# Kernel tuning notes

Hardware: AMD Instinct MI355X
Metric: run time of the kernel (lower is better)

The kernel has to match this reference:

```python
import jax, jax.numpy as jnp
import numpy as np

B, S, D = 2, 4096, 2048
HEADS, HEAD_DIM = 16, 128
EPS = 1e-5


def setup_inputs() -> dict:
    key = jax.random.key(0)
    ks = jax.random.split(key, 8)
    hidden_states = jax.random.normal(ks[0], (B, S, D), dtype=jnp.float32)
    # rotary angles, broadcastable to [B, S, heads, head_dim]
    freqs_cis = jax.random.uniform(ks[1], (1, S, 1, HEAD_DIM), dtype=jnp.float32) * 6.283185
    scale = 1.0 / np.sqrt(D)
    # weights stored [in, out] (transpose of torch Linear weight)
    wq = jax.random.normal(ks[2], (D, HEADS * HEAD_DIM), dtype=jnp.float32) * scale
    wk = jax.random.normal(ks[3], (D, HEADS * HEAD_DIM), dtype=jnp.float32) * scale
    wv = jax.random.normal(ks[4], (D, HEADS * HEAD_DIM), dtype=jnp.float32) * scale
    norm_q_w = jnp.ones((HEAD_DIM,), dtype=jnp.float32)
    norm_k_w = jnp.ones((HEAD_DIM,), dtype=jnp.float32)
    w_out = jax.random.normal(ks[5], (HEADS * HEAD_DIM, D), dtype=jnp.float32) * scale
    b_out = jnp.zeros((D,), dtype=jnp.float32)
    return {"hidden_states": hidden_states, "freqs_cis": freqs_cis,
            "wq": wq, "wk": wk, "wv": wv,
            "norm_q_w": norm_q_w, "norm_k_w": norm_k_w,
            "w_out": w_out, "b_out": b_out}


def _rms_norm(x, w):
    var = jnp.mean(jnp.square(x), axis=-1, keepdims=True)
    return x * jax.lax.rsqrt(var + EPS) * w


def _apply_rotary(x, freqs_cis):
    rot_dim = freqs_cis.shape[-1]
    xr, x_pass = x[..., :rot_dim], x[..., rot_dim:]
    cos_ = jnp.cos(freqs_cis).astype(x.dtype)
    sin_ = jnp.sin(freqs_cis).astype(x.dtype)
    x1, x2 = jnp.split(xr, 2, axis=-1)
    x_rot = jnp.concatenate((-x2, x1), axis=-1)
    return jnp.concatenate((xr * cos_ + x_rot * sin_, x_pass), axis=-1)


def reference(hidden_states, freqs_cis, wq, wk, wv, norm_q_w, norm_k_w, w_out, b_out):
    b, s, _ = hidden_states.shape
    # QKV projections -> [B, S, H, Dh]
    q = (hidden_states @ wq).reshape(b, s, HEADS, HEAD_DIM)
    k = (hidden_states @ wk).reshape(b, s, HEADS, HEAD_DIM)
    v = (hidden_states @ wv).reshape(b, s, HEADS, HEAD_DIM)
    q = _rms_norm(q, norm_q_w)
    k = _rms_norm(k, norm_k_w)
    q = _apply_rotary(q, freqs_cis)
    k = _apply_rotary(k, freqs_cis)
    # SDPA with BSND layout, scale = 1/sqrt(head_dim)
    attn = jax.nn.dot_product_attention(q, k, v)  # [B, S, H, Dh]
    out = attn.reshape(b, s, HEADS * HEAD_DIM) @ w_out + b_out
    return out
```

## Files before the change

kernel.cpp:

```cpp
#include <hip/hip_runtime.h>
#include <stdint.h>


#define S_LEN  4096
#define NHEAD  16
#define HDIM   128
#define DMODEL 2048
#define MROWS  8192

typedef unsigned short u16;
typedef unsigned int   u32;
typedef __attribute__((ext_vector_type(4)))  float  f32x4;
typedef __attribute__((ext_vector_type(16))) float  f32x16;
typedef __attribute__((ext_vector_type(4)))  u16    u16x4;
typedef __attribute__((ext_vector_type(8)))  u16    u16x8;
typedef __attribute__((ext_vector_type(4)))  u32    u32x4;
typedef __attribute__((ext_vector_type(8)))  __bf16 bf16x8;

__device__ __forceinline__ u16 f2bf(float x){
  unsigned u = __builtin_bit_cast(unsigned, x);
  u += 0x7FFFu + ((u >> 16) & 1u);
  return (u16)(u >> 16);
}
__device__ __forceinline__ float bf2f(u16 b){
  unsigned u = ((unsigned)b) << 16;
  return __builtin_bit_cast(float, u);
}
__device__ __forceinline__ u32 cvtpk(float lo, float hi_){
  u32 r;
  asm("v_cvt_pk_bf16_f32 %0, %1, %2" : "=v"(r) : "v"(lo), "v"(hi_));
  return r;
}
__device__ __forceinline__ void gload16(const void* g, void* l){
  __builtin_amdgcn_global_load_lds((__attribute__((address_space(1))) void*)g,
                                   (__attribute__((address_space(3))) void*)l,
                                   16, 0, 0);
}
__device__ __forceinline__ int xcd_chunk(int bid, int nwg){
  return (bid & 7) * (nwg >> 3) + (bid >> 3);
}

__global__ void k_cast_hs(const float* __restrict__ in, u16* __restrict__ out){
  size_t i = (size_t)blockIdx.x * 256 + threadIdx.x;
  const f32x4* p = (const f32x4*)in;
  f32x4 a = p[i*2], b = p[i*2+1];
  u16x8 o;
  o[0]=f2bf(a[0]); o[1]=f2bf(a[1]); o[2]=f2bf(a[2]); o[3]=f2bf(a[3]);
  o[4]=f2bf(b[0]); o[5]=f2bf(b[1]); o[6]=f2bf(b[2]); o[7]=f2bf(b[3]);
  ((u16x8*)out)[i] = o;
}

__global__ void k_transpose_w(const float* __restrict__ in, u16* __restrict__ out){
  __shared__ float t[64][65];
  const int tid = threadIdx.x;
  const int k0 = blockIdx.x * 64, n0 = blockIdx.y * 64;
#pragma unroll
  for (int it = 0; it < 4; ++it){
    int slot = it*256 + tid;
    int r = slot >> 4, c = (slot & 15) * 4;
    f32x4 v = *(const f32x4*)&in[(size_t)(k0+r)*DMODEL + n0 + c];
    t[r][c] = v[0]; t[r][c+1] = v[1]; t[r][c+2] = v[2]; t[r][c+3] = v[3];
  }
  __syncthreads();
#pragma unroll
  for (int it = 0; it < 2; ++it){
    int slot = it*256 + tid;
    int r = slot >> 3, c = (slot & 7) * 8;
    u16x8 o;
#pragma unroll
    for (int j = 0; j < 8; ++j) o[j] = f2bf(t[c+j][r]);
    *(u16x8*)&out[(size_t)(n0+r)*DMODEL + k0 + c] = o;
  }
}

__global__ void k_tables(const float* __restrict__ fr, float* __restrict__ cn,
                         float* __restrict__ sn){
  int i = blockIdx.x*256 + threadIdx.x;
  float f = fr[i];
  cn[i] = cosf(f); sn[i] = sinf(f);
}

__device__ __forceinline__ void gemm_loop(const u16* __restrict__ A,
                                          const u16* __restrict__ Bt,
                                          int m0, int n0,
                                          u16* Asm, u16* Bsm,
                                          f32x4 (&acc)[4][4], int lane, int wid){
  const int wr = wid >> 1, wc = wid & 1;
#pragma unroll 1
  for (int kt = 0; kt < DMODEL/64; ++kt){
#pragma unroll
    for (int it = 0; it < 4; ++it){
      int slot = it*256 + wid*64 + lane;
      int row = slot >> 3, cs = slot & 7;
      int ci = cs ^ (row & 7);
      gload16(A  + (size_t)(m0+row)*DMODEL + kt*64 + ci*8, Asm + (size_t)(it*256 + wid*64)*8);
      gload16(Bt + (size_t)(n0+row)*DMODEL + kt*64 + ci*8, Bsm + (size_t)(it*256 + wid*64)*8);
    }
    __syncthreads();
#pragma unroll
    for (int ks = 0; ks < 2; ++ks){
      bf16x8 af[4], bfv[4];
#pragma unroll
      for (int mt = 0; mt < 4; ++mt){
        int row = wr*64 + mt*16 + (lane & 15);
        int cs = (ks*4 + (lane >> 4)) ^ (row & 7);
        af[mt] = *(const bf16x8*)(Asm + ((size_t)row*8 + cs)*8);
      }
#pragma unroll
      for (int nt = 0; nt < 4; ++nt){
        int row = wc*64 + nt*16 + (lane & 15);
        int cs = (ks*4 + (lane >> 4)) ^ (row & 7);
        bfv[nt] = *(const bf16x8*)(Bsm + ((size_t)row*8 + cs)*8);
      }
#pragma unroll
      for (int mt = 0; mt < 4; ++mt)
#pragma unroll
        for (int nt = 0; nt < 4; ++nt)
          acc[mt][nt] = __builtin_amdgcn_mfma_f32_16x16x32_bf16(af[mt], bfv[nt], acc[mt][nt], 0, 0, 0);
    }
    __syncthreads();
  }
}

__global__ __launch_bounds__(256, 2)
void k_gemm_qkv(const u16* __restrict__ A, const u16* __restrict__ Bt,
                u16* __restrict__ qkp, u16* __restrict__ vt){
  __shared__ u16 Asm[128*64];
  __shared__ u16 Bsm[128*64];
  const int lane = threadIdx.x & 63, wid = threadIdx.x >> 6;
  const int m0 = blockIdx.x * 128, n0 = blockIdx.y * 128;
  f32x4 acc[4][4] = {};
  gemm_loop(A, Bt, m0, n0, Asm, Bsm, acc, lane, wid);
  const int wr = wid >> 1, wc = wid & 1;
  if (n0 < 2*DMODEL){
#pragma unroll
    for (int mt = 0; mt < 4; ++mt)
#pragma unroll
      for (int nt = 0; nt < 4; ++nt){
        int col = n0 + wc*64 + nt*16 + (lane & 15);
#pragma unroll
        for (int r = 0; r < 4; ++r){
          int row = m0 + wr*64 + mt*16 + (lane >> 4)*4 + r;
          qkp[(size_t)row*4096 + col] = f2bf(acc[mt][nt][r]);
        }
      }
  } else {
    const int hh = (n0 - 2*DMODEL) >> 7;
    const int b  = m0 >> 12;
#pragma unroll
    for (int mt = 0; mt < 4; ++mt)
#pragma unroll
      for (int nt = 0; nt < 4; ++nt){
        u16x4 pk;
#pragma unroll
        for (int r = 0; r < 4; ++r) pk[r] = f2bf(acc[mt][nt][r]);
        int d  = wc*64 + nt*16 + (lane & 15);
        int s_ = (m0 & (S_LEN-1)) + wr*64 + mt*16 + (lane >> 4)*4;
        *(u16x4*)&vt[(((size_t)b*NHEAD + hh)*HDIM + d)*S_LEN + s_] = pk;
      }
  }
}

__global__ __launch_bounds__(256)
void k_qk_post(const u16* __restrict__ qkp, const float* __restrict__ cn,
               const float* __restrict__ sn, const float* __restrict__ wqn,
               const float* __restrict__ wkn, u16* __restrict__ Qo, u16* __restrict__ Ko){
  const int lane = threadIdx.x & 63, wid = threadIdx.x >> 6;
  const int gw = blockIdx.x*4 + wid;
  const int row = gw >> 4;
  const int h  = gw & 15;
  const int s_ = row & (S_LEN-1);
  const int b  = row >> 12;
  const float c1 = cn[s_*HDIM + lane],      c2 = cn[s_*HDIM + 64 + lane];
  const float t1 = sn[s_*HDIM + lane],      t2 = sn[s_*HDIM + 64 + lane];
  const size_t ob = (((size_t)b*NHEAD + h)*S_LEN + s_)*HDIM;
  {
    const u16* p = qkp + (size_t)row*4096 + h*HDIM;
    float x1 = bf2f(p[lane]), x2 = bf2f(p[lane+64]);
    float ss = x1*x1 + x2*x2;
#pragma unroll
    for (int m = 1; m < 64; m <<= 1) ss += __shfl_xor(ss, m);
    float rn = rsqrtf(ss*(1.0f/128.0f) + 1e-5f);
    x1 *= rn * wqn[lane]; x2 *= rn * wqn[lane+64];
    const float qs = 0.12751743f;
    Qo[ob + lane]      = f2bf((x1*c1 - x2*t1) * qs);
    Qo[ob + 64 + lane] = f2bf((x2*c2 + x1*t2) * qs);
  }
  {
    const u16* p = qkp + (size_t)row*4096 + 2048 + h*HDIM;
    float x1 = bf2f(p[lane]), x2 = bf2f(p[lane+64]);
    float ss = x1*x1 + x2*x2;
#pragma unroll
    for (int m = 1; m < 64; m <<= 1) ss += __shfl_xor(ss, m);
    float rn = rsqrtf(ss*(1.0f/128.0f) + 1e-5f);
    x1 *= rn * wkn[lane]; x2 *= rn * wkn[lane+64];
    Ko[ob + lane]      = f2bf(x1*c1 - x2*t1);
    Ko[ob + 64 + lane] = f2bf(x2*c2 + x1*t2);
  }
}

__device__ __forceinline__ void stage_kv(const u16* __restrict__ Kg,
                                         const u16* __restrict__ Vt,
                                         size_t base, int kb,
                                         u16* Ksm, u16* Vsm, int lane, int wid){
#pragma unroll
  for (int it = 0; it < 4; ++it){
    int slot = it*256 + wid*64 + lane;
    { int row = slot >> 4, cs = slot & 15, ci = cs ^ (row & 7);
      gload16(Kg + base + (size_t)(kb*64 + row)*HDIM + ci*8, Ksm + (size_t)(it*256 + wid*64)*8); }
    { int row = slot >> 3, cs = slot & 7,  ci = cs ^ (row & 7);
      gload16(Vt + base + (size_t)row*S_LEN + kb*64 + ci*8,  Vsm + (size_t)(it*256 + wid*64)*8); }
  }
}

__global__ __launch_bounds__(256, 2)
void k_attn(const u16* __restrict__ Q, const u16* __restrict__ Kg,
            const u16* __restrict__ Vt, u16* __restrict__ Og){
  __shared__ u16 Ksm[2][64*128];
  __shared__ u16 Vsm[2][128*64];
  const int lane = threadIdx.x & 63, wid = threadIdx.x >> 6;
  const int col = lane & 31, hi = lane >> 5;
  const int t  = xcd_chunk(blockIdx.x, 1024);
  const int bh = t >> 5;
  const int q0 = (t & 31) * 128;
  const int b = bh >> 4, h = bh & 15;
  const size_t base = (size_t)bh * S_LEN * HDIM;
  const int qw = q0 + wid*32;

  stage_kv(Kg, Vt, base, 0, Ksm[0], Vsm[0], lane, wid);

  bf16x8 qb[8];
  {
    const u16* qp = Q + base + (size_t)(qw + col)*HDIM + hi*8;
#pragma unroll
    for (int ks = 0; ks < 8; ++ks) qb[ks] = *(const bf16x8*)(qp + ks*16);
  }
  f32x16 acc[4] = {};
  float lsum = 0.f;
  int cur = 0;

#pragma unroll 1
  for (int kb = 0; kb < S_LEN/64; ++kb){
    if (kb + 1 < S_LEN/64){
      stage_kv(Kg, Vt, base, kb + 1, Ksm[cur ^ 1], Vsm[cur ^ 1], lane, wid);
      asm volatile("s_waitcnt vmcnt(8)" ::: "memory");
    } else {
      asm volatile("s_waitcnt vmcnt(0)" ::: "memory");
    }
    __builtin_amdgcn_s_barrier();
    asm volatile("" ::: "memory");
    const u16* Ks = Ksm[cur];
    const u16* Vs = Vsm[cur];

    f32x16 s0 = {}, s1 = {};
    __builtin_amdgcn_s_setprio(1);
#pragma unroll
    for (int ks = 0; ks < 8; ++ks){
      int slot = (ks*2 + hi);
      int r0 = col;
      bf16x8 kf0 = *(const bf16x8*)(Ks + (size_t)r0*128 + (size_t)(slot ^ (r0 & 7))*8);
      s0 = __builtin_amdgcn_mfma_f32_32x32x16_bf16(kf0, qb[ks], s0, 0, 0, 0);
      int r1 = col + 32;
      bf16x8 kf1 = *(const bf16x8*)(Ks + (size_t)r1*128 + (size_t)(slot ^ (r1 & 7))*8);
      s1 = __builtin_amdgcn_mfma_f32_32x32x16_bf16(kf1, qb[ks], s1, 0, 0, 0);
    }
    __builtin_amdgcn_s_setprio(0);

    float p0[16], p1[16];
#pragma unroll
    for (int r = 0; r < 16; ++r){
      p0[r] = __builtin_amdgcn_exp2f(s0[r]);
      p1[r] = __builtin_amdgcn_exp2f(s1[r]);
      lsum += p0[r] + p1[r];
    }
    u32 cw0[8], cw1[8];
#pragma unroll
    for (int j = 0; j < 8; ++j){
      cw0[j] = cvtpk(p0[2*j], p0[2*j+1]);
      cw1[j] = cvtpk(p1[2*j], p1[2*j+1]);
    }
    bf16x8 pa[4];
#pragma unroll
    for (int ks = 0; ks < 4; ++ks){
      const u32* cw = (ks < 2) ? cw0 : cw1;
      const int c4 = (ks & 1) * 4;
      u32 n0 = hi ? cw[c4+2] : cw[c4+0];
      u32 n1 = hi ? cw[c4+3] : cw[c4+1];
      u32 s0w = hi ? cw[c4+0] : cw[c4+2];
      u32 s1w = hi ? cw[c4+1] : cw[c4+3];
      u32 f0 = __shfl_xor((int)s0w, 32);
      u32 f1 = __shfl_xor((int)s1w, 32);
      u32x4 w;
      w[0] = hi ? f0 : n0;
      w[1] = hi ? f1 : n1;
      w[2] = hi ? n0 : f0;
      w[3] = hi ? n1 : f1;
      pa[ks] = __builtin_bit_cast(bf16x8, w);
    }

    __builtin_amdgcn_s_setprio(1);
#pragma unroll
    for (int dt = 0; dt < 4; ++dt){
      int row = dt*32 + col;
      const u16* vb = Vs + (size_t)row*64;
      int sw = row & 7;
#pragma unroll
      for (int ks = 0; ks < 4; ++ks){
        bf16x8 vf = *(const bf16x8*)(vb + (size_t)((ks*2 + hi) ^ sw)*8);
        acc[dt] = __builtin_amdgcn_mfma_f32_32x32x16_bf16(pa[ks], vf, acc[dt], 0, 0, 0);
      }
    }
    __builtin_amdgcn_s_setprio(0);
    __builtin_amdgcn_s_barrier();
    asm volatile("" ::: "memory");
    cur ^= 1;
  }

  float tot = lsum + __shfl_xor(lsum, 32);
  float inv[16];
#pragma unroll
  for (int r = 0; r < 16; ++r){
    int qr = (r & 3) + 4*hi + 8*(r >> 2);
    inv[r] = 1.0f / __shfl(tot, qr);
  }
  const size_t orow0 = (size_t)b*S_LEN + q0 + wid*32;
#pragma unroll
  for (int dt = 0; dt < 4; ++dt){
    int d = h*HDIM + dt*32 + col;
#pragma unroll
    for (int r = 0; r < 16; ++r){
      int qr = (r & 3) + 4*hi + 8*(r >> 2);
      Og[(orow0 + qr)*DMODEL + d] = f2bf(acc[dt][r] * inv[r]);
    }
  }
}

__global__ __launch_bounds__(256, 2)
void k_gemm_out(const u16* __restrict__ A, const u16* __restrict__ Bt,
                const float* __restrict__ bias, float* __restrict__ out){
  __shared__ u16 Asm[128*64];
  __shared__ u16 Bsm[128*64];
  const int lane = threadIdx.x & 63, wid = threadIdx.x >> 6;
  const int m0 = blockIdx.x * 128, n0 = blockIdx.y * 128;
  f32x4 acc[4][4] = {};
  gemm_loop(A, Bt, m0, n0, Asm, Bsm, acc, lane, wid);
  const int wr = wid >> 1, wc = wid & 1;
  float bv[4];
#pragma unroll
  for (int nt = 0; nt < 4; ++nt) bv[nt] = bias[n0 + wc*64 + nt*16 + (lane & 15)];
#pragma unroll
  for (int mt = 0; mt < 4; ++mt)
#pragma unroll
    for (int nt = 0; nt < 4; ++nt){
      int col = n0 + wc*64 + nt*16 + (lane & 15);
#pragma unroll
      for (int r = 0; r < 4; ++r){
        int row = m0 + wr*64 + mt*16 + (lane >> 4)*4 + r;
        out[(size_t)row*DMODEL + col] = acc[mt][nt][r] + bv[nt];
      }
    }
}

extern "C" void kernel_launch(void* const* d_in, const int* in_sizes, int n_in,
                              void* d_out, int out_size, void* d_ws, size_t ws_size,
                              hipStream_t stream){
  const float* hs    = (const float*)d_in[0];
  const float* freqs = (const float*)d_in[1];
  const float* wq    = (const float*)d_in[2];
  const float* wk    = (const float*)d_in[3];
  const float* wv    = (const float*)d_in[4];
  const float* nqw   = (const float*)d_in[5];
  const float* nkw   = (const float*)d_in[6];
  const float* wo    = (const float*)d_in[7];
  const float* bo    = (const float*)d_in[8];
  float* out = (float*)d_out;

  char* ws = (char*)d_ws;
  u16*   hs_bf = (u16*)(ws + 0);
  u16*   wqkvT = (u16*)(ws + 33554432);
  u16*   woutT = (u16*)(ws + 58720256);
  float* cosn  = (float*)(ws + 67108864);
  float* sinn  = (float*)(ws + 69206016);
  u16*   qkp   = (u16*)(ws + 71303168);
  u16*   vt    = (u16*)(ws + 138412032);
  u16*   kbuf  = (u16*)(ws + 171966464);
  if (ws_size < 205520896ULL) return;
  u16* qbuf = hs_bf;
  u16* attn = qkp;

  k_cast_hs    <<<8192, 256, 0, stream>>>(hs, hs_bf);
  k_transpose_w<<<dim3(32,32), 256, 0, stream>>>(wq, wqkvT);
  k_transpose_w<<<dim3(32,32), 256, 0, stream>>>(wk, wqkvT + (size_t)DMODEL*DMODEL);
  k_transpose_w<<<dim3(32,32), 256, 0, stream>>>(wv, wqkvT + (size_t)2*DMODEL*DMODEL);
  k_transpose_w<<<dim3(32,32), 256, 0, stream>>>(wo, woutT);
  k_tables     <<<2048, 256, 0, stream>>>(freqs, cosn, sinn);
  k_gemm_qkv   <<<dim3(64,48), 256, 0, stream>>>(hs_bf, wqkvT, qkp, vt);
  k_qk_post    <<<32768, 256, 0, stream>>>(qkp, cosn, sinn, nqw, nkw, qbuf, kbuf);
  k_attn       <<<1024, 256, 0, stream>>>(qbuf, kbuf, vt, attn);
  k_gemm_out   <<<dim3(64,16), 256, 0, stream>>>(attn, woutT, bo, out);
}
```

Before: 641.9 us.

## Rewrite projection GEMMs as 256x256 double-buffered pipelined 8-wave tiles

Replaces the 128x128 single-buffer GEMM loop used by the QKV and output projections with a 256x256 tile, 8-wave kernel. Global-to-LDS loads are split into half-tiles and double-buffered so they overlap the MFMA work, with explicit vmcnt waits, barriers and setprio around the MFMA bursts. Blocks are remapped through xcd_chunk for L2 locality across XCDs. The larger tile raises data reuse, but the 128 KB of LDS and heavier register use may cut occupancy, and only 256 blocks are launched for the output GEMM.

```diff
diff --git a/kernel.cpp b/kernel.cpp
--- a/kernel.cpp
+++ b/kernel.cpp
@@ -7,6 +7,8 @@
 #define HDIM   128
 #define DMODEL 2048
 #define MROWS  8192
+#define NT     (DMODEL/64)
+#define NI     (NT/2)
 
 typedef unsigned short u16;
 typedef unsigned int   u32;
@@ -80,82 +82,155 @@
   cn[i] = cosf(f); sn[i] = sinf(f);
 }
 
-__device__ __forceinline__ void gemm_loop(const u16* __restrict__ A,
-                                          const u16* __restrict__ Bt,
-                                          int m0, int n0,
-                                          u16* Asm, u16* Bsm,
-                                          f32x4 (&acc)[4][4], int lane, int wid){
-  const int wr = wid >> 1, wc = wid & 1;
+
+__device__ __forceinline__ void stage_Ah(const u16* __restrict__ A, int m0, int kt,
+                                         int h, u16* dst, int lane, int wid){
+#pragma unroll
+  for (int r = 0; r < 2; ++r){
+    int lr0 = r*64 + wid*8;
+    int rb  = (lr0 < 64) ? (h*64 + lr0) : (128 + h*64 + (lr0 - 64));
+    int row = rb + (lane >> 3), cs = lane & 7, ci = cs ^ (row & 7);
+    gload16(A + (size_t)(m0+row)*DMODEL + kt*64 + ci*8, dst + (size_t)rb*64);
+  }
+}
+__device__ __forceinline__ void stage_Bh(const u16* __restrict__ Bt, int n0, int kt,
+                                         int h, u16* dst, int lane, int wid){
+#pragma unroll
+  for (int r = 0; r < 2; ++r){
+    int lr0 = r*64 + wid*8;
+    int rb  = (lr0 >> 5)*64 + h*32 + (lr0 & 31);
+    int row = rb + (lane >> 3), cs = lane & 7, ci = cs ^ (row & 7);
+    gload16(Bt + (size_t)(n0+row)*DMODEL + kt*64 + ci*8, dst + (size_t)rb*64);
+  }
+}
+
+struct Frags { bf16x8 af[4][2]; bf16x8 bv[2][2]; };
+
+__device__ __forceinline__ void ld_frags(const u16* As, const u16* Bs, int mh, int nh,
+                                         int lane, int wr, int wc, Frags& f){
+#pragma unroll
+  for (int mr = 0; mr < 4; ++mr){
+    int row = wr*128 + mh*64 + mr*16 + (lane & 15);
+    int sw = row & 7;
+#pragma unroll
+    for (int ks = 0; ks < 2; ++ks)
+      f.af[mr][ks] = *(const bf16x8*)(As + (size_t)row*64 + (size_t)((ks*4 + (lane>>4)) ^ sw)*8);
+  }
+#pragma unroll
+  for (int nr = 0; nr < 2; ++nr){
+    int row = wc*64 + nh*32 + nr*16 + (lane & 15);
+    int sw = row & 7;
+#pragma unroll
+    for (int ks = 0; ks < 2; ++ks)
+      f.bv[nr][ks] = *(const bf16x8*)(Bs + (size_t)row*64 + (size_t)((ks*4 + (lane>>4)) ^ sw)*8);
+  }
+}
+
+__device__ __forceinline__ void do_mfma(Frags& f, f32x4 (&acc)[8][4], int mh, int nh, int vm){
+  asm volatile("" ::: "memory");
+  __builtin_amdgcn_s_barrier();
+  asm volatile("" ::: "memory");
+  __builtin_amdgcn_s_setprio(1);
+#pragma unroll
+  for (int mr = 0; mr < 4; ++mr)
+#pragma unroll
+    for (int nr = 0; nr < 2; ++nr)
+#pragma unroll
+      for (int ks = 0; ks < 2; ++ks)
+        acc[mh*4+mr][nh*2+nr] = __builtin_amdgcn_mfma_f32_16x16x32_bf16(
+            f.af[mr][ks], f.bv[nr][ks], acc[mh*4+mr][nh*2+nr], 0, 0, 0);
+  __builtin_amdgcn_s_setprio(0);
+  if (vm == 2)      asm volatile("s_waitcnt vmcnt(2)" ::: "memory");
+  else if (vm == 0) asm volatile("s_waitcnt vmcnt(0)" ::: "memory");
+  __builtin_amdgcn_sched_barrier(0);
+  asm volatile("" ::: "memory");
+  __builtin_amdgcn_s_barrier();
+  asm volatile("" ::: "memory");
+}
+
+__device__ __forceinline__ void gemm8p(const u16* __restrict__ A, const u16* __restrict__ Bt,
+                                       int m0, int n0,
+                                       u16 (*Asm)[256*64], u16 (*Bsm)[256*64],
+                                       f32x4 (&acc)[8][4], int lane, int wid){
+  const int wr = wid >> 2, wc = wid & 3;
+  stage_Ah(A,  m0, 0, 0, Asm[0], lane, wid);
+  stage_Ah(A,  m0, 0, 1, Asm[0], lane, wid);
+  stage_Bh(Bt, n0, 0, 0, Bsm[0], lane, wid);
+  stage_Bh(Bt, n0, 0, 1, Bsm[0], lane, wid);
+  stage_Bh(Bt, n0, 1, 0, Bsm[1], lane, wid);
+  asm volatile("s_waitcnt vmcnt(2)" ::: "memory");
+  __builtin_amdgcn_s_barrier();
+  asm volatile("" ::: "memory");
+
+  Frags f;
 #pragma unroll 1
-  for (int kt = 0; kt < DMODEL/64; ++kt){
-#pragma unroll
-    for (int it = 0; it < 4; ++it){
-      int slot = it*256 + wid*64 + lane;
-      int row = slot >> 3, cs = slot & 7;
-      int ci = cs ^ (row & 7);
-      gload16(A  + (size_t)(m0+row)*DMODEL + kt*64 + ci*8, Asm + (size_t)(it*256 + wid*64)*8);
-      gload16(Bt + (size_t)(n0+row)*DMODEL + kt*64 + ci*8, Bsm + (size_t)(it*256 + wid*64)*8);
-    }
-    __syncthreads();
-#pragma unroll
-    for (int ks = 0; ks < 2; ++ks){
-      bf16x8 af[4], bfv[4];
-#pragma unroll
-      for (int mt = 0; mt < 4; ++mt){
-        int row = wr*64 + mt*16 + (lane & 15);
-        int cs = (ks*4 + (lane >> 4)) ^ (row & 7);
-        af[mt] = *(const bf16x8*)(Asm + ((size_t)row*8 + cs)*8);
-      }
-#pragma unroll
-      for (int nt = 0; nt < 4; ++nt){
-        int row = wc*64 + nt*16 + (lane & 15);
-        int cs = (ks*4 + (lane >> 4)) ^ (row & 7);
-        bfv[nt] = *(const bf16x8*)(Bsm + ((size_t)row*8 + cs)*8);
-      }
-#pragma unroll
-      for (int mt = 0; mt < 4; ++mt)
-#pragma unroll
-        for (int nt = 0; nt < 4; ++nt)
-          acc[mt][nt] = __builtin_amdgcn_mfma_f32_16x16x32_bf16(af[mt], bfv[nt], acc[mt][nt], 0, 0, 0);
-    }
-    __syncthreads();
-  }
-}
-
-__global__ __launch_bounds__(256, 2)
+  for (int I = 0; I < NI; ++I){
+    const int t = 2*I;
+    const bool last = (I == NI-1);
+    ld_frags(Asm[0], Bsm[0], 0, 0, lane, wr, wc, f);
+    stage_Ah(A,  m0, t+1, 0, Asm[1], lane, wid);
+    do_mfma(f, acc, 0, 0, -1);
+    ld_frags(Asm[0], Bsm[0], 1, 0, lane, wr, wc, f);
+    stage_Ah(A,  m0, t+1, 1, Asm[1], lane, wid);
+    do_mfma(f, acc, 1, 0, -1);
+    ld_frags(Asm[0], Bsm[0], 0, 1, lane, wr, wc, f);
+    stage_Bh(Bt, n0, t+1, 1, Bsm[1], lane, wid);
+    do_mfma(f, acc, 0, 1, -1);
+    ld_frags(Asm[0], Bsm[0], 1, 1, lane, wr, wc, f);
+    if (!last) stage_Bh(Bt, n0, t+2, 0, Bsm[0], lane, wid);
+    do_mfma(f, acc, 1, 1, last ? 0 : 2);
+    ld_frags(Asm[1], Bsm[1], 0, 0, lane, wr, wc, f);
+    if (!last) stage_Ah(A,  m0, t+2, 0, Asm[0], lane, wid);
+    do_mfma(f, acc, 0, 0, -1);
+    ld_frags(Asm[1], Bsm[1], 1, 0, lane, wr, wc, f);
+    if (!last) stage_Ah(A,  m0, t+2, 1, Asm[0], lane, wid);
+    do_mfma(f, acc, 1, 0, -1);
+    ld_frags(Asm[1], Bsm[1], 0, 1, lane, wr, wc, f);
+    if (!last) stage_Bh(Bt, n0, t+2, 1, Bsm[0], lane, wid);
+    do_mfma(f, acc, 0, 1, -1);
+    ld_frags(Asm[1], Bsm[1], 1, 1, lane, wr, wc, f);
+    if (!last) stage_Bh(Bt, n0, t+3, 0, Bsm[1], lane, wid);
+    do_mfma(f, acc, 1, 1, last ? -1 : 2);
+  }
+}
+
+__global__ __launch_bounds__(512, 2)
 void k_gemm_qkv(const u16* __restrict__ A, const u16* __restrict__ Bt,
                 u16* __restrict__ qkp, u16* __restrict__ vt){
-  __shared__ u16 Asm[128*64];
-  __shared__ u16 Bsm[128*64];
+  __shared__ u16 Asm[2][256*64];
+  __shared__ u16 Bsm[2][256*64];
   const int lane = threadIdx.x & 63, wid = threadIdx.x >> 6;
-  const int m0 = blockIdx.x * 128, n0 = blockIdx.y * 128;
-  f32x4 acc[4][4] = {};
-  gemm_loop(A, Bt, m0, n0, Asm, Bsm, acc, lane, wid);
-  const int wr = wid >> 1, wc = wid & 1;
+  const int t  = xcd_chunk(blockIdx.x, 32*24);
+  const int m0 = (t & 31) * 256;
+  const int n0 = (t >> 5) * 256;
+  f32x4 acc[8][4] = {};
+  gemm8p(A, Bt, m0, n0, Asm, Bsm, acc, lane, wid);
+  const int wr = wid >> 2, wc = wid & 3;
   if (n0 < 2*DMODEL){
 #pragma unroll
-    for (int mt = 0; mt < 4; ++mt)
-#pragma unroll
-      for (int nt = 0; nt < 4; ++nt){
-        int col = n0 + wc*64 + nt*16 + (lane & 15);
+    for (int mg = 0; mg < 8; ++mg)
+#pragma unroll
+      for (int ng = 0; ng < 4; ++ng){
+        int col = n0 + wc*64 + ng*16 + (lane & 15);
 #pragma unroll
         for (int r = 0; r < 4; ++r){
-          int row = m0 + wr*64 + mt*16 + (lane >> 4)*4 + r;
-          qkp[(size_t)row*4096 + col] = f2bf(acc[mt][nt][r]);
+          int row = m0 + wr*128 + mg*16 + (lane >> 4)*4 + r;
+          qkp[(size_t)row*4096 + col] = f2bf(acc[mg][ng][r]);
         }
       }
   } else {
-    const int hh = (n0 - 2*DMODEL) >> 7;
-    const int b  = m0 >> 12;
-#pragma unroll
-    for (int mt = 0; mt < 4; ++mt)
-#pragma unroll
-      for (int nt = 0; nt < 4; ++nt){
+    const int b = m0 >> 12;
+#pragma unroll
+    for (int mg = 0; mg < 8; ++mg)
+#pragma unroll
+      for (int ng = 0; ng < 4; ++ng){
+        int ncol = n0 + wc*64 + ng*16 + (lane & 15);
+        int hh = (ncol >> 7) & 15;
+        int d  = ncol & 127;
         u16x4 pk;
 #pragma unroll
-        for (int r = 0; r < 4; ++r) pk[r] = f2bf(acc[mt][nt][r]);
-        int d  = wc*64 + nt*16 + (lane & 15);
-        int s_ = (m0 & (S_LEN-1)) + wr*64 + mt*16 + (lane >> 4)*4;
+        for (int r = 0; r < 4; ++r) pk[r] = f2bf(acc[mg][ng][r]);
+        int s_ = (m0 & (S_LEN-1)) + wr*128 + mg*16 + (lane >> 4)*4;
         *(u16x4*)&vt[(((size_t)b*NHEAD + hh)*HDIM + d)*S_LEN + s_] = pk;
       }
   }
@@ -335,28 +410,28 @@
   }
 }
 
-__global__ __launch_bounds__(256, 2)
+__global__ __launch_bounds__(512, 2)
 void k_gemm_out(const u16* __restrict__ A, const u16* __restrict__ Bt,
                 const float* __restrict__ bias, float* __restrict__ out){
-  __shared__ u16 Asm[128*64];
-  __shared__ u16 Bsm[128*64];
+  __shared__ u16 Asm[2][256*64];
+  __shared__ u16 Bsm[2][256*64];
   const int lane = threadIdx.x & 63, wid = threadIdx.x >> 6;
-  const int m0 = blockIdx.x * 128, n0 = blockIdx.y * 128;
-  f32x4 acc[4][4] = {};
-  gemm_loop(A, Bt, m0, n0, Asm, Bsm, acc, lane, wid);
-  const int wr = wid >> 1, wc = wid & 1;
-  float bv[4];
-#pragma unroll
-  for (int nt = 0; nt < 4; ++nt) bv[nt] = bias[n0 + wc*64 + nt*16 + (lane & 15)];
-#pragma unroll
-  for (int mt = 0; mt < 4; ++mt)
-#pragma unroll
-    for (int nt = 0; nt < 4; ++nt){
-      int col = n0 + wc*64 + nt*16 + (lane & 15);
+  const int t  = xcd_chunk(blockIdx.x, 32*8);
+  const int m0 = (t & 31) * 256;
+  const int n0 = (t >> 5) * 256;
+  f32x4 acc[8][4] = {};
+  gemm8p(A, Bt, m0, n0, Asm, Bsm, acc, lane, wid);
+  const int wr = wid >> 2, wc = wid & 3;
+#pragma unroll
+  for (int mg = 0; mg < 8; ++mg)
+#pragma unroll
+    for (int ng = 0; ng < 4; ++ng){
+      int col = n0 + wc*64 + ng*16 + (lane & 15);
+      float bv = bias[col];
 #pragma unroll
       for (int r = 0; r < 4; ++r){
-        int row = m0 + wr*64 + mt*16 + (lane >> 4)*4 + r;
-        out[(size_t)row*DMODEL + col] = acc[mt][nt][r] + bv[nt];
+        int row = m0 + wr*128 + mg*16 + (lane >> 4)*4 + r;
+        out[(size_t)row*DMODEL + col] = acc[mg][ng][r] + bv;
       }
     }
 }
@@ -394,8 +469,8 @@
   k_transpose_w<<<dim3(32,32), 256, 0, stream>>>(wv, wqkvT + (size_t)2*DMODEL*DMODEL);
   k_transpose_w<<<dim3(32,32), 256, 0, stream>>>(wo, woutT);
   k_tables     <<<2048, 256, 0, stream>>>(freqs, cosn, sinn);
-  k_gemm_qkv   <<<dim3(64,48), 256, 0, stream>>>(hs_bf, wqkvT, qkp, vt);
+  k_gemm_qkv   <<<768, 512, 0, stream>>>(hs_bf, wqkvT, qkp, vt);
   k_qk_post    <<<32768, 256, 0, stream>>>(qkp, cosn, sinn, nqw, nkw, qbuf, kbuf);
   k_attn       <<<1024, 256, 0, stream>>>(qbuf, kbuf, vt, attn);
-  k_gemm_out   <<<dim3(64,16), 256, 0, stream>>>(attn, woutT, bo, out);
-}
+  k_gemm_out   <<<256, 512, 0, stream>>>(attn, woutT, bo, out);
+}
```

Result: slower. 664.4 us (+3.5%).

## Single-buffer V tile and issue its load after PV to cut LDS

Applied to the files above, without the earlier changes.

V is now single-buffered while K stays double-buffered. The next V tile is loaded after the trailing barrier of each iteration, so it overlaps the next K prefetch and the QK^T MFMAs. This frees 16KB of LDS per block, which may improve occupancy. In exchange, the V load has less time to hide latency before it is needed in the following iteration.

```diff
diff --git a/kernel.cpp b/kernel.cpp
--- a/kernel.cpp
+++ b/kernel.cpp
@@ -199,17 +199,22 @@
   }
 }
 
-__device__ __forceinline__ void stage_kv(const u16* __restrict__ Kg,
-                                         const u16* __restrict__ Vt,
-                                         size_t base, int kb,
-                                         u16* Ksm, u16* Vsm, int lane, int wid){
+__device__ __forceinline__ void stage_k(const u16* __restrict__ Kg, size_t base, int kb,
+                                        u16* Ksm, int lane, int wid){
 #pragma unroll
   for (int it = 0; it < 4; ++it){
     int slot = it*256 + wid*64 + lane;
-    { int row = slot >> 4, cs = slot & 15, ci = cs ^ (row & 7);
-      gload16(Kg + base + (size_t)(kb*64 + row)*HDIM + ci*8, Ksm + (size_t)(it*256 + wid*64)*8); }
-    { int row = slot >> 3, cs = slot & 7,  ci = cs ^ (row & 7);
-      gload16(Vt + base + (size_t)row*S_LEN + kb*64 + ci*8,  Vsm + (size_t)(it*256 + wid*64)*8); }
+    int row = slot >> 4, cs = slot & 15, ci = cs ^ (row & 7);
+    gload16(Kg + base + (size_t)(kb*64 + row)*HDIM + ci*8, Ksm + (size_t)(it*256 + wid*64)*8);
+  }
+}
+__device__ __forceinline__ void stage_v(const u16* __restrict__ Vt, size_t base, int kb,
+                                        u16* Vsm, int lane, int wid){
+#pragma unroll
+  for (int it = 0; it < 4; ++it){
+    int slot = it*256 + wid*64 + lane;
+    int row = slot >> 3, cs = slot & 7, ci = cs ^ (row & 7);
+    gload16(Vt + base + (size_t)row*S_LEN + kb*64 + ci*8, Vsm + (size_t)(it*256 + wid*64)*8);
   }
 }
 
@@ -217,7 +222,7 @@
 void k_attn(const u16* __restrict__ Q, const u16* __restrict__ Kg,
             const u16* __restrict__ Vt, u16* __restrict__ Og){
   __shared__ u16 Ksm[2][64*128];
-  __shared__ u16 Vsm[2][128*64];
+  __shared__ u16 Vsm[128*64];
   const int lane = threadIdx.x & 63, wid = threadIdx.x >> 6;
   const int col = lane & 31, hi = lane >> 5;
   const int t  = xcd_chunk(blockIdx.x, 1024);
@@ -226,8 +231,10 @@
   const int b = bh >> 4, h = bh & 15;
   const size_t base = (size_t)bh * S_LEN * HDIM;
   const int qw = q0 + wid*32;
-
-  stage_kv(Kg, Vt, base, 0, Ksm[0], Vsm[0], lane, wid);
+  const int NT = S_LEN/64;
+
+  stage_k(Kg, base, 0, Ksm[0], lane, wid);
+  stage_v(Vt, base, 0, Vsm,    lane, wid);
 
   bf16x8 qb[8];
   {
@@ -237,20 +244,19 @@
   }
   f32x16 acc[4] = {};
   float lsum = 0.f;
-  int cur = 0;
 
 #pragma unroll 1
-  for (int kb = 0; kb < S_LEN/64; ++kb){
-    if (kb + 1 < S_LEN/64){
-      stage_kv(Kg, Vt, base, kb + 1, Ksm[cur ^ 1], Vsm[cur ^ 1], lane, wid);
-      asm volatile("s_waitcnt vmcnt(8)" ::: "memory");
+  for (int kb = 0; kb < NT; ++kb){
+    if (kb + 1 < NT){
+      stage_k(Kg, base, kb + 1, Ksm[(kb + 1) & 1], lane, wid);
+      asm volatile("s_waitcnt vmcnt(4)" ::: "memory");
     } else {
       asm volatile("s_waitcnt vmcnt(0)" ::: "memory");
     }
     __builtin_amdgcn_s_barrier();
     asm volatile("" ::: "memory");
-    const u16* Ks = Ksm[cur];
-    const u16* Vs = Vsm[cur];
+    const u16* Ks = Ksm[kb & 1];
+    const u16* Vs = Vsm;
 
     f32x16 s0 = {}, s1 = {};
     __builtin_amdgcn_s_setprio(1);
@@ -313,7 +319,8 @@
     __builtin_amdgcn_s_setprio(0);
     __builtin_amdgcn_s_barrier();
     asm volatile("" ::: "memory");
-    cur ^= 1;
+    if (kb + 1 < NT)
+      stage_v(Vt, base, kb + 1, Vsm, lane, wid);
   }
 
   float tot = lsum + __shfl_xor(lsum, 32);
```

After: 647.6 us. About the same (+0.9%).
